# Kernel optimization log

Hardware: AMD Instinct MI355X
Metric: run time of the kernel (lower is better)

The kernel has to match this reference:

```python
import jax, jax.numpy as jnp
import numpy as np
import math


def setup_inputs() -> dict:
    key = jax.random.key(0)
    ks = jax.random.split(key, 6)
    B, C, H, W = 4, 384, 64, 64
    nd = 12
    d = C // nd  # 32 = projected channel width
    return {
        "x": jax.random.normal(ks[0], (B, C, H, W), jnp.float32),
        "xe": jax.random.normal(ks[1], (B, C, H, W), jnp.float32),
        "Wq": jax.random.normal(ks[2], (d, C), jnp.float32) * 0.02,      # 1x1 conv C -> d, no bias
        "Wkv": jax.random.normal(ks[3], (2 * d, C), jnp.float32) * 0.02,  # 1x1 conv C -> 2d, no bias
        "Wout": jax.random.normal(ks[4], (C, d, 3, 3), jnp.float32) * 0.02,  # 3x3 conv d -> C
        "bout": jnp.zeros((C,), jnp.float32),
        "n_div": 12,
    }


def reference(x, xe, Wq, Wkv, Wout, bout, n_div):
    B, C, H, W = x.shape
    Y, X = xe.shape[-2], xe.shape[-1]
    n_head = 1
    hd = C // (n_head * n_div)  # head_dim
    # 1x1 conv projections as einsums
    q = jnp.einsum('dc,bchw->bdhw', Wq, x).reshape(B, n_head, hd, H, W)
    kv = jnp.einsum('dc,bchw->bdhw', Wkv, xe).reshape(B, n_head, 2 * hd, Y, X)
    k, v = kv[:, :, :hd], kv[:, :, hd:]
    # full pairwise spatial attention scores [B, n_head, H, W, Y, X]
    scale = 1.0 / math.sqrt(C // n_div)
    attn = jnp.einsum('bnchw,bncyx->bnhwyx', q, k) * scale
    attn = jax.nn.softmax(attn.reshape(B, n_head, H, W, Y * X), axis=-1)
    attn = attn.reshape(B, n_head, H, W, Y, X)
    out = jnp.einsum('bnhwyx,bncyx->bnchw', attn, v).reshape(B, C // n_div, H, W)
    # 3x3 conv with padding 1, plus bias, then residual
    out = jax.lax.conv_general_dilated(
        out, Wout, window_strides=(1, 1), padding='SAME',
        dimension_numbers=('NCHW', 'OIHW', 'NCHW'))
    out = out + bout[None, :, None, None]
    return out + x
```

## Files before the change

kernel.cpp:

```cpp
#include <hip/hip_runtime.h>
#include <hip/hip_bf16.h>
#include <math.h>

#define B_   4
#define C_   384
#define HD_  32
#define P_   4096
#define PADP 4356
#define SCALE_ 0.17677669529663687f

typedef __attribute__((ext_vector_type(4))) float f32x4;
typedef __attribute__((ext_vector_type(8))) short short8;

static __device__ inline unsigned pk_bf16(float a, float b) {
    __hip_bfloat16 x = __float2bfloat16(a), y = __float2bfloat16(b);
    unsigned short ux = *reinterpret_cast<unsigned short*>(&x);
    unsigned short uy = *reinterpret_cast<unsigned short*>(&y);
    return (unsigned)ux | ((unsigned)uy << 16);
}
static __device__ inline short bf16_bits(float a) {
    __hip_bfloat16 x = __float2bfloat16(a);
    return *reinterpret_cast<short*>(&x);
}

__global__ void zero_kernel(f32x4* __restrict__ p, int n16) {
    int i = blockIdx.x * 256 + threadIdx.x;
    if (i < n16) p[i] = (f32x4){0.f, 0.f, 0.f, 0.f};
}

__global__ void repack_wproj_kernel(const float* __restrict__ Wq,
                                    const float* __restrict__ Wkv,
                                    short* __restrict__ Wball) {
    int idx = blockIdx.x * 256 + threadIdx.x;
    if (idx >= 96 * C_) return;
    int r = idx / C_, c = idx % C_;
    float v = (r < 32) ? Wq[r * C_ + c] : Wkv[(r - 32) * C_ + c];
    Wball[idx] = bf16_bits(v);
}

__global__ void repack_wconv_kernel(const float* __restrict__ Wout,
                                    short* __restrict__ Wbc) {
    int idx = blockIdx.x * 256 + threadIdx.x;
    if (idx >= 9 * 384 * 32) return;
    int ci = idx & 31;
    int co = (idx >> 5) % 384;
    int kk = idx / (384 * 32);
    int ky = kk / 3, kx = kk % 3;
    Wbc[idx] = bf16_bits(Wout[((co * 32 + ci) * 3 + ky) * 3 + kx]);
}

__global__ __launch_bounds__(256)
void transpose_kernel(const float* __restrict__ in, short* __restrict__ outT) {
    __shared__ float ls[64][65];
    int ct = blockIdx.x >> 6;
    int pt = blockIdx.x & 63;
    int b  = blockIdx.y;
    int c0 = ct << 6, p0 = pt << 6;
    int t = threadIdx.x;
    {
        int cc = t >> 2, pb = (t & 3) << 4;
        const float* src = in + ((size_t)b * C_ + c0 + cc) * P_ + p0 + pb;
        float4 v0 = *(const float4*)(src);
        float4 v1 = *(const float4*)(src + 4);
        float4 v2 = *(const float4*)(src + 8);
        float4 v3 = *(const float4*)(src + 12);
        float* d = &ls[cc][pb];
        d[0]=v0.x; d[1]=v0.y; d[2]=v0.z; d[3]=v0.w;
        d[4]=v1.x; d[5]=v1.y; d[6]=v1.z; d[7]=v1.w;
        d[8]=v2.x; d[9]=v2.y; d[10]=v2.z; d[11]=v2.w;
        d[12]=v3.x; d[13]=v3.y; d[14]=v3.z; d[15]=v3.w;
    }
    __syncthreads();
    {
        int p = t >> 2, cb = (t & 3) << 4;
        unsigned pkv[8];
        #pragma unroll
        for (int j = 0; j < 8; ++j)
            pkv[j] = pk_bf16(ls[cb + 2 * j][p], ls[cb + 2 * j + 1][p]);
        unsigned* dst = (unsigned*)(outT + ((size_t)b * P_ + p0 + p) * C_ + c0 + cb);
        #pragma unroll
        for (int j = 0; j < 8; ++j) dst[j] = pkv[j];
    }
}

__global__ __launch_bounds__(256)
void proj_gemm_kernel(const short* __restrict__ inT, const short* __restrict__ Wball,
                      short* __restrict__ pmOut, short* __restrict__ vOut, int role0) {
    int role = role0 + blockIdx.z;
    int b = blockIdx.y;
    int p0 = blockIdx.x << 6;
    int t = threadIdx.x, w = t >> 6, l = t & 63, lq = l & 15, h = l >> 4;
    int p = p0 + w * 16 + lq;
    const short* Ap = Wball + (size_t)(role * 32 + lq) * C_ + h * 8;
    const short* Bp = inT + ((size_t)b * P_ + p) * C_ + h * 8;
    f32x4 acc0 = {0.f,0.f,0.f,0.f}, acc1 = {0.f,0.f,0.f,0.f};
    short8 a0 = *(const short8*)(Ap);
    short8 a1 = *(const short8*)(Ap + 16 * C_);
    short8 bb = *(const short8*)(Bp);
    #pragma unroll
    for (int ks = 0; ks < 11; ++ks) {
        const short* Ap2 = Ap + (ks + 1) * 32;
        short8 na0 = *(const short8*)(Ap2);
        short8 na1 = *(const short8*)(Ap2 + 16 * C_);
        short8 nbb = *(const short8*)(Bp + (ks + 1) * 32);
        acc0 = __builtin_amdgcn_mfma_f32_16x16x32_bf16(a0, bb, acc0, 0, 0, 0);
        acc1 = __builtin_amdgcn_mfma_f32_16x16x32_bf16(a1, bb, acc1, 0, 0, 0);
        a0 = na0; a1 = na1; bb = nbb;
    }
    acc0 = __builtin_amdgcn_mfma_f32_16x16x32_bf16(a0, bb, acc0, 0, 0, 0);
    acc1 = __builtin_amdgcn_mfma_f32_16x16x32_bf16(a1, bb, acc1, 0, 0, 0);

    if (role < 2) {
        uint2 u0, u1;
        u0.x = pk_bf16(acc0[0], acc0[1]); u0.y = pk_bf16(acc0[2], acc0[3]);
        u1.x = pk_bf16(acc1[0], acc1[1]); u1.y = pk_bf16(acc1[2], acc1[3]);
        *(uint2*)(pmOut + ((size_t)b * P_ + p) * HD_ + h * 4)      = u0;
        *(uint2*)(pmOut + ((size_t)b * P_ + p) * HD_ + 16 + h * 4) = u1;
    } else {
        #pragma unroll
        for (int r = 0; r < 4; ++r) {
            vOut[((size_t)b * HD_ + h * 4 + r) * P_ + p]      = bf16_bits(acc0[r]);
            vOut[((size_t)b * HD_ + 16 + h * 4 + r) * P_ + p] = bf16_bits(acc1[r]);
        }
    }
}

__global__ __launch_bounds__(256, 4)
void attn_mfma_kernel(const short* __restrict__ qT,
                      const short* __restrict__ kT,
                      const short* __restrict__ vT,
                      short* __restrict__ aoT) {
    __shared__ unsigned p_lds[4][512];
    __shared__ float o_lds[4][32][16];
    __shared__ float m_lds[4][16], l_lds[4][16];

    int blk = blockIdx.x;
    int b = blk >> 8;
    int q0 = (blk & 255) << 4;
    int t = threadIdx.x;
    int w = t >> 6;
    int l = t & 63;
    int lq = l & 15;
    int h = l >> 4;

    const short* qTb = qT + ((size_t)b * P_ + q0) * HD_;
    const short* kTb = kT + (size_t)b * P_ * HD_;
    const short* vb  = vT + (size_t)b * HD_ * P_;

    short8 qf = *(const short8*)(qTb + lq * HD_ + h * 8);

    f32x4 o0 = {0.f,0.f,0.f,0.f}, o1 = {0.f,0.f,0.f,0.f};
    float m = -1e30f, lsum = 0.f;
    unsigned* myp = &p_lds[w][0];
    int swz = (lq & 7) << 4;

    int key_base = w * 1024;
    short8 kf[4], vf[4];
    {
        const short* kp = kTb + (size_t)(key_base + lq) * HD_ + h * 8;
        #pragma unroll
        for (int tt = 0; tt < 4; ++tt) kf[tt] = *(const short8*)(kp + tt * 16 * HD_);
        const short* vp = vb + (size_t)lq * P_ + key_base + h * 8;
        vf[0] = *(const short8*)(vp);
        vf[1] = *(const short8*)(vp + 32);
        vf[2] = *(const short8*)(vp + 16 * P_);
        vf[3] = *(const short8*)(vp + 16 * P_ + 32);
    }

    for (int kt = 0; kt < 16; ++kt) {
        short8 nk[4], nv[4];
        if (kt < 15) {
            int nxt = key_base + (kt + 1) * 64;
            const short* kp = kTb + (size_t)(nxt + lq) * HD_ + h * 8;
            #pragma unroll
            for (int tt = 0; tt < 4; ++tt) nk[tt] = *(const short8*)(kp + tt * 16 * HD_);
            const short* vp = vb + (size_t)lq * P_ + nxt + h * 8;
            nv[0] = *(const short8*)(vp);
            nv[1] = *(const short8*)(vp + 32);
            nv[2] = *(const short8*)(vp + 16 * P_);
            nv[3] = *(const short8*)(vp + 16 * P_ + 32);
        } else {
            #pragma unroll
            for (int tt = 0; tt < 4; ++tt) { nk[tt] = kf[tt]; nv[tt] = vf[tt]; }
        }

        f32x4 st[4];
        __builtin_amdgcn_s_setprio(1);
        #pragma unroll
        for (int tt = 0; tt < 4; ++tt)
            st[tt] = __builtin_amdgcn_mfma_f32_16x16x32_bf16(kf[tt], qf,
                         (f32x4){0.f,0.f,0.f,0.f}, 0, 0, 0);
        __builtin_amdgcn_s_setprio(0);

        float pm = -1e30f;
        #pragma unroll
        for (int tt = 0; tt < 4; ++tt)
            #pragma unroll
            for (int r = 0; r < 4; ++r) pm = fmaxf(pm, st[tt][r]);
        pm *= SCALE_;
        pm = fmaxf(pm, __shfl_xor(pm, 16));
        pm = fmaxf(pm, __shfl_xor(pm, 32));

        bool skip = __all(pm - m <= 8.0f);
        if (!skip) {
            float mnew = fmaxf(m, pm);
            float alpha = __expf(m - mnew);
            o0 *= alpha; o1 *= alpha;
            lsum *= alpha;
            m = mnew;
        }

        float rs = 0.f;
        unsigned pk[8];
        #pragma unroll
        for (int tt = 0; tt < 4; ++tt) {
            float p0e = __expf(st[tt][0] * SCALE_ - m);
            float p1e = __expf(st[tt][1] * SCALE_ - m);
            float p2e = __expf(st[tt][2] * SCALE_ - m);
            float p3e = __expf(st[tt][3] * SCALE_ - m);
            rs += p0e + p1e + p2e + p3e;
            pk[tt * 2 + 0] = pk_bf16(p0e, p1e);
            pk[tt * 2 + 1] = pk_bf16(p2e, p3e);
        }
        rs += __shfl_xor(rs, 16);
        rs += __shfl_xor(rs, 32);
        lsum += rs;

        #pragma unroll
        for (int tt = 0; tt < 4; ++tt) {
            int u0 = tt * 32 + h * 8;
            myp[(lq * 128 + ((u0 + 0) ^ swz)) >> 2] = pk[tt * 2 + 0];
            myp[(lq * 128 + ((u0 + 4) ^ swz)) >> 2] = pk[tt * 2 + 1];
        }
        short8 pb0, pb1;
        __builtin_memcpy(&pb0, (const char*)myp + lq * 128 + ((h * 16 + 0)  ^ swz), 16);
        __builtin_memcpy(&pb1, (const char*)myp + lq * 128 + ((h * 16 + 64) ^ swz), 16);

        __builtin_amdgcn_s_setprio(1);
        o0 = __builtin_amdgcn_mfma_f32_16x16x32_bf16(vf[0], pb0, o0, 0, 0, 0);
        o0 = __builtin_amdgcn_mfma_f32_16x16x32_bf16(vf[1], pb1, o0, 0, 0, 0);
        o1 = __builtin_amdgcn_mfma_f32_16x16x32_bf16(vf[2], pb0, o1, 0, 0, 0);
        o1 = __builtin_amdgcn_mfma_f32_16x16x32_bf16(vf[3], pb1, o1, 0, 0, 0);
        __builtin_amdgcn_s_setprio(0);

        #pragma unroll
        for (int tt = 0; tt < 4; ++tt) { kf[tt] = nk[tt]; vf[tt] = nv[tt]; }
    }

    #pragma unroll
    for (int r = 0; r < 4; ++r) {
        o_lds[w][h * 4 + r][lq]      = o0[r];
        o_lds[w][16 + h * 4 + r][lq] = o1[r];
    }
    if (h == 0) { m_lds[w][lq] = m; l_lds[w][lq] = lsum; }
    __syncthreads();

    {
        int qq = t >> 4;
        int d0 = (t & 15) * 2;
        float M = fmaxf(fmaxf(m_lds[0][qq], m_lds[1][qq]),
                        fmaxf(m_lds[2][qq], m_lds[3][qq]));
        float f[4]; float denom = 0.f;
        #pragma unroll
        for (int ww = 0; ww < 4; ++ww) {
            f[ww] = __expf(m_lds[ww][qq] - M);
            denom += l_lds[ww][qq] * f[ww];
        }
        float inv = 1.f / denom;
        float v0 = 0.f, v1 = 0.f;
        #pragma unroll
        for (int ww = 0; ww < 4; ++ww) {
            v0 += o_lds[ww][d0][qq] * f[ww];
            v1 += o_lds[ww][d0 + 1][qq] * f[ww];
        }
        int p = q0 + qq;
        int hh = p >> 6, ww2 = p & 63;
        unsigned* dst = (unsigned*)(aoT +
            ((size_t)b * PADP + (hh + 1) * 66 + (ww2 + 1)) * HD_ + d0);
        *dst = pk_bf16(v0 * inv, v1 * inv);
    }
}

__global__ __launch_bounds__(512)
void conv_mfma_kernel(const short* __restrict__ Wbc,
                      const short* __restrict__ aoT,
                      const float* __restrict__ bout,
                      const float* __restrict__ x,
                      float* __restrict__ out) {
    int blk = blockIdx.x;
    int b = blk >> 7;
    int p0 = (blk & 127) << 5;
    int t = threadIdx.x;
    int w = t >> 6, l = t & 63, lq = l & 15, h = l >> 4;
    int co0 = w * 48;

    const short* aob = aoT + (size_t)b * PADP * HD_;
    const short* bptr[2];
    #pragma unroll
    for (int n = 0; n < 2; ++n) {
        int p = p0 + n * 16 + lq;
        int hh = p >> 6, ww = p & 63;
        bptr[n] = aob + (size_t)(hh * 66 + ww) * HD_ + h * 8;
    }
    const short* aptr = Wbc + (size_t)(co0 + lq) * 32 + h * 8;

    f32x4 acc[3][2];
    #pragma unroll
    for (int m = 0; m < 3; ++m)
        #pragma unroll
        for (int n = 0; n < 2; ++n) acc[m][n] = (f32x4){0.f,0.f,0.f,0.f};

    short8 Bf0 = *(const short8*)(bptr[0]);
    short8 Bf1 = *(const short8*)(bptr[1]);
    #pragma unroll
    for (int kk = 0; kk < 9; ++kk) {
        short8 nB0, nB1;
        if (kk < 8) {
            int ky = (kk + 1) / 3, kx = (kk + 1) % 3;
            nB0 = *(const short8*)(bptr[0] + (ky * 66 + kx) * HD_);
            nB1 = *(const short8*)(bptr[1] + (ky * 66 + kx) * HD_);
        } else { nB0 = Bf0; nB1 = Bf1; }
        #pragma unroll
        for (int m = 0; m < 3; ++m) {
            short8 Af = *(const short8*)(aptr + kk * 12288 + m * 512);
            acc[m][0] = __builtin_amdgcn_mfma_f32_16x16x32_bf16(Af, Bf0, acc[m][0], 0, 0, 0);
            acc[m][1] = __builtin_amdgcn_mfma_f32_16x16x32_bf16(Af, Bf1, acc[m][1], 0, 0, 0);
        }
        Bf0 = nB0; Bf1 = nB1;
    }

    #pragma unroll
    for (int m = 0; m < 3; ++m) {
        #pragma unroll
        for (int r = 0; r < 4; ++r) {
            int co = co0 + m * 16 + h * 4 + r;
            float bias = bout[co];
            #pragma unroll
            for (int n = 0; n < 2; ++n) {
                int p = p0 + n * 16 + lq;
                size_t idx = ((size_t)b * C_ + co) * P_ + p;
                out[idx] = acc[m][n][r] + bias + x[idx];
            }
        }
    }
}

extern "C" void kernel_launch(void* const* d_in, const int* in_sizes, int n_in,
                              void* d_out, int out_size, void* d_ws, size_t ws_size,
                              hipStream_t stream) {
    const float* x    = (const float*)d_in[0];
    const float* xe   = (const float*)d_in[1];
    const float* Wq   = (const float*)d_in[2];
    const float* Wkv  = (const float*)d_in[3];
    const float* Wout = (const float*)d_in[4];
    const float* bout = (const float*)d_in[5];
    float* out = (float*)d_out;

    short* iT    = (short*)d_ws;
    short* qT    = iT    + (size_t)B_ * P_ * C_;
    short* kT    = qT    + (size_t)B_ * P_ * HD_;
    short* vT    = kT    + (size_t)B_ * P_ * HD_;
    short* aoT   = vT    + (size_t)B_ * P_ * HD_;
    short* Wball = aoT   + (size_t)B_ * PADP * HD_;
    short* Wbc   = Wball + 96 * C_;

    {
        int n16 = (B_ * PADP * HD_ * 2) / 16;
        zero_kernel<<<(n16 + 255) / 256, 256, 0, stream>>>((f32x4*)aoT, n16);
    }
    repack_wproj_kernel<<<(96 * C_ + 255) / 256, 256, 0, stream>>>(Wq, Wkv, Wball);
    repack_wconv_kernel<<<(9 * 384 * 32 + 255) / 256, 256, 0, stream>>>(Wout, Wbc);

    transpose_kernel<<<dim3(384, B_), 256, 0, stream>>>(xe, iT);
    proj_gemm_kernel<<<dim3(64, B_, 2), 256, 0, stream>>>(iT, Wball, kT, vT, 1);
    transpose_kernel<<<dim3(384, B_), 256, 0, stream>>>(x, iT);
    proj_gemm_kernel<<<dim3(64, B_, 1), 256, 0, stream>>>(iT, Wball, qT, vT, 0);

    attn_mfma_kernel<<<B_ * 256, 256, 0, stream>>>(qT, kT, vT, aoT);
    conv_mfma_kernel<<<B_ * 128, 512, 0, stream>>>(Wbc, aoT, bout, x, out);
}
```

Measured before the change: 108.4 us.

## Fuse projections into attention, drop transposes, use exp2 with prescaled Q

Removes the two fp32→bf16 transpose kernels. K/V are now projected straight from the NCHW input with strided loads and an in-register bf16 pack, and the Q projection is computed inside the attention kernel itself. The softmax scale and log2(e) are folded into Wq, so attention can use the raw v_exp_f32 (exp2) instruction. Attention moves to 8 waves per block with 32-key steps, split-K over 512 keys per wave, and keeps the row-sum local until the end. Several small launches are merged and only the padded border of aoT is zeroed, trading strided uncoalesced input reads and Q recomputation for less launch and memory traffic.

```diff
diff --git a/kernel.cpp b/kernel.cpp
--- a/kernel.cpp
+++ b/kernel.cpp
@@ -8,244 +8,201 @@
 #define P_   4096
 #define PADP 4356
 #define SCALE_ 0.17677669529663687f
+#define QSC_   0.2550889266f
 
 typedef __attribute__((ext_vector_type(4))) float f32x4;
 typedef __attribute__((ext_vector_type(8))) short short8;
 
-static __device__ inline unsigned pk_bf16(float a, float b) {
-    __hip_bfloat16 x = __float2bfloat16(a), y = __float2bfloat16(b);
-    unsigned short ux = *reinterpret_cast<unsigned short*>(&x);
-    unsigned short uy = *reinterpret_cast<unsigned short*>(&y);
-    return (unsigned)ux | ((unsigned)uy << 16);
+static __device__ inline unsigned cvt_pk(float lo, float hi) {
+    unsigned r;
+    asm("v_cvt_pk_bf16_f32 %0, %1, %2" : "=v"(r) : "v"(lo), "v"(hi));
+    return r;
+}
+static __device__ inline float exp2a(float x) {
+    float r;
+    asm("v_exp_f32 %0, %1" : "=v"(r) : "v"(x));
+    return r;
 }
 static __device__ inline short bf16_bits(float a) {
     __hip_bfloat16 x = __float2bfloat16(a);
     return *reinterpret_cast<short*>(&x);
 }
 
-__global__ void zero_kernel(f32x4* __restrict__ p, int n16) {
-    int i = blockIdx.x * 256 + threadIdx.x;
-    if (i < n16) p[i] = (f32x4){0.f, 0.f, 0.f, 0.f};
-}
-
-__global__ void repack_wproj_kernel(const float* __restrict__ Wq,
-                                    const float* __restrict__ Wkv,
-                                    short* __restrict__ Wball) {
+__global__ void border_zero_kernel(unsigned* __restrict__ aoT32) {
     int idx = blockIdx.x * 256 + threadIdx.x;
-    if (idx >= 96 * C_) return;
-    int r = idx / C_, c = idx % C_;
-    float v = (r < 32) ? Wq[r * C_ + c] : Wkv[(r - 32) * C_ + c];
-    Wball[idx] = bf16_bits(v);
-}
-
-__global__ void repack_wconv_kernel(const float* __restrict__ Wout,
-                                    short* __restrict__ Wbc) {
+    if (idx >= B_ * 260 * 16) return;
+    int j = idx & 15;
+    int p = (idx >> 4) % 260;
+    int b = idx / (260 * 16);
+    int hh, ww;
+    if (p < 66)       { hh = 0;  ww = p; }
+    else if (p < 132) { hh = 65; ww = p - 66; }
+    else { int i = p - 132; hh = 1 + (i >> 1); ww = (i & 1) * 65; }
+    aoT32[((size_t)b * PADP + hh * 66 + ww) * 16 + j] = 0;
+}
+
+__global__ void repack_kernel(const float* __restrict__ Wq,
+                              const float* __restrict__ Wkv,
+                              const float* __restrict__ Wout,
+                              short* __restrict__ Wball,
+                              short* __restrict__ Wbc) {
     int idx = blockIdx.x * 256 + threadIdx.x;
-    if (idx >= 9 * 384 * 32) return;
-    int ci = idx & 31;
-    int co = (idx >> 5) % 384;
-    int kk = idx / (384 * 32);
-    int ky = kk / 3, kx = kk % 3;
-    Wbc[idx] = bf16_bits(Wout[((co * 32 + ci) * 3 + ky) * 3 + kx]);
-}
-
-__global__ __launch_bounds__(256)
-void transpose_kernel(const float* __restrict__ in, short* __restrict__ outT) {
-    __shared__ float ls[64][65];
-    int ct = blockIdx.x >> 6;
-    int pt = blockIdx.x & 63;
-    int b  = blockIdx.y;
-    int c0 = ct << 6, p0 = pt << 6;
-    int t = threadIdx.x;
-    {
-        int cc = t >> 2, pb = (t & 3) << 4;
-        const float* src = in + ((size_t)b * C_ + c0 + cc) * P_ + p0 + pb;
-        float4 v0 = *(const float4*)(src);
-        float4 v1 = *(const float4*)(src + 4);
-        float4 v2 = *(const float4*)(src + 8);
-        float4 v3 = *(const float4*)(src + 12);
-        float* d = &ls[cc][pb];
-        d[0]=v0.x; d[1]=v0.y; d[2]=v0.z; d[3]=v0.w;
-        d[4]=v1.x; d[5]=v1.y; d[6]=v1.z; d[7]=v1.w;
-        d[8]=v2.x; d[9]=v2.y; d[10]=v2.z; d[11]=v2.w;
-        d[12]=v3.x; d[13]=v3.y; d[14]=v3.z; d[15]=v3.w;
-    }
-    __syncthreads();
-    {
-        int p = t >> 2, cb = (t & 3) << 4;
-        unsigned pkv[8];
-        #pragma unroll
-        for (int j = 0; j < 8; ++j)
-            pkv[j] = pk_bf16(ls[cb + 2 * j][p], ls[cb + 2 * j + 1][p]);
-        unsigned* dst = (unsigned*)(outT + ((size_t)b * P_ + p0 + p) * C_ + c0 + cb);
-        #pragma unroll
-        for (int j = 0; j < 8; ++j) dst[j] = pkv[j];
-    }
-}
-
-__global__ __launch_bounds__(256)
-void proj_gemm_kernel(const short* __restrict__ inT, const short* __restrict__ Wball,
-                      short* __restrict__ pmOut, short* __restrict__ vOut, int role0) {
-    int role = role0 + blockIdx.z;
+    if (idx < 96 * C_) {
+        int r = idx / C_, c = idx % C_;
+        float v = (r < 32) ? Wq[r * C_ + c] * QSC_ : Wkv[(r - 32) * C_ + c];
+        Wball[idx] = bf16_bits(v);
+    }
+    int j = idx - 96 * C_;
+    if (j >= 0 && j < 9 * 384 * 32) {
+        int ci = j & 31;
+        int co = (j >> 5) % 384;
+        int kk = j / (384 * 32);
+        int ky = kk / 3, kx = kk % 3;
+        Wbc[j] = bf16_bits(Wout[((co * 32 + ci) * 3 + ky) * 3 + kx]);
+    }
+}
+
+__global__ __launch_bounds__(512)
+void proj_kv_kernel(const float* __restrict__ xe, const short* __restrict__ Wball,
+                    short* __restrict__ kT, short* __restrict__ vT) {
     int b = blockIdx.y;
-    int p0 = blockIdx.x << 6;
+    int p0 = blockIdx.x << 5;
     int t = threadIdx.x, w = t >> 6, l = t & 63, lq = l & 15, h = l >> 4;
-    int p = p0 + w * 16 + lq;
-    const short* Ap = Wball + (size_t)(role * 32 + lq) * C_ + h * 8;
-    const short* Bp = inT + ((size_t)b * P_ + p) * C_ + h * 8;
-    f32x4 acc0 = {0.f,0.f,0.f,0.f}, acc1 = {0.f,0.f,0.f,0.f};
-    short8 a0 = *(const short8*)(Ap);
-    short8 a1 = *(const short8*)(Ap + 16 * C_);
-    short8 bb = *(const short8*)(Bp);
-    #pragma unroll
-    for (int ks = 0; ks < 11; ++ks) {
-        const short* Ap2 = Ap + (ks + 1) * 32;
-        short8 na0 = *(const short8*)(Ap2);
-        short8 na1 = *(const short8*)(Ap2 + 16 * C_);
-        short8 nbb = *(const short8*)(Bp + (ks + 1) * 32);
-        acc0 = __builtin_amdgcn_mfma_f32_16x16x32_bf16(a0, bb, acc0, 0, 0, 0);
-        acc1 = __builtin_amdgcn_mfma_f32_16x16x32_bf16(a1, bb, acc1, 0, 0, 0);
-        a0 = na0; a1 = na1; bb = nbb;
-    }
-    acc0 = __builtin_amdgcn_mfma_f32_16x16x32_bf16(a0, bb, acc0, 0, 0, 0);
-    acc1 = __builtin_amdgcn_mfma_f32_16x16x32_bf16(a1, bb, acc1, 0, 0, 0);
-
-    if (role < 2) {
-        uint2 u0, u1;
-        u0.x = pk_bf16(acc0[0], acc0[1]); u0.y = pk_bf16(acc0[2], acc0[3]);
-        u1.x = pk_bf16(acc1[0], acc1[1]); u1.y = pk_bf16(acc1[2], acc1[3]);
-        *(uint2*)(pmOut + ((size_t)b * P_ + p) * HD_ + h * 4)      = u0;
-        *(uint2*)(pmOut + ((size_t)b * P_ + p) * HD_ + 16 + h * 4) = u1;
+    int mt = w >> 1, pg = w & 1;
+    int p = p0 + pg * 16 + lq;
+    const float* xb = xe + (size_t)b * C_ * P_ + p;
+    const short* Ap = Wball + (size_t)(32 + mt * 16 + lq) * C_ + h * 8;
+    f32x4 acc = {0.f, 0.f, 0.f, 0.f};
+    for (int ks = 0; ks < 12; ++ks) {
+        float xv[8];
+        #pragma unroll
+        for (int jj = 0; jj < 8; ++jj)
+            xv[jj] = xb[(size_t)(ks * 32 + h * 8 + jj) * P_];
+        unsigned u[4];
+        #pragma unroll
+        for (int jj = 0; jj < 4; ++jj) u[jj] = cvt_pk(xv[2 * jj], xv[2 * jj + 1]);
+        short8 bf;
+        __builtin_memcpy(&bf, u, 16);
+        short8 af = *(const short8*)(Ap + ks * 32);
+        acc = __builtin_amdgcn_mfma_f32_16x16x32_bf16(af, bf, acc, 0, 0, 0);
+    }
+    if (mt < 2) {
+        uint2 u;
+        u.x = cvt_pk(acc[0], acc[1]);
+        u.y = cvt_pk(acc[2], acc[3]);
+        *(uint2*)(kT + ((size_t)b * P_ + p) * HD_ + mt * 16 + h * 4) = u;
     } else {
-        #pragma unroll
-        for (int r = 0; r < 4; ++r) {
-            vOut[((size_t)b * HD_ + h * 4 + r) * P_ + p]      = bf16_bits(acc0[r]);
-            vOut[((size_t)b * HD_ + 16 + h * 4 + r) * P_ + p] = bf16_bits(acc1[r]);
-        }
-    }
-}
-
-__global__ __launch_bounds__(256, 4)
-void attn_mfma_kernel(const short* __restrict__ qT,
-                      const short* __restrict__ kT,
-                      const short* __restrict__ vT,
+        int d = (mt - 2) * 16 + h * 4;
+        #pragma unroll
+        for (int r = 0; r < 4; ++r)
+            vT[((size_t)b * HD_ + d + r) * P_ + p] = bf16_bits(acc[r]);
+    }
+}
+
+__global__ __launch_bounds__(512, 8)
+void attn_mfma_kernel(const float* __restrict__ x, const short* __restrict__ Wball,
+                      const short* __restrict__ kT, const short* __restrict__ vT,
                       short* __restrict__ aoT) {
-    __shared__ unsigned p_lds[4][512];
-    __shared__ float o_lds[4][32][16];
-    __shared__ float m_lds[4][16], l_lds[4][16];
+    __shared__ unsigned p_lds[8][256];
+    __shared__ float o_lds[8][32][16];
+    __shared__ float m_lds[8][16], l_lds[8][16];
 
     int blk = blockIdx.x;
     int b = blk >> 8;
     int q0 = (blk & 255) << 4;
-    int t = threadIdx.x;
-    int w = t >> 6;
-    int l = t & 63;
-    int lq = l & 15;
-    int h = l >> 4;
-
-    const short* qTb = qT + ((size_t)b * P_ + q0) * HD_;
+    int t = threadIdx.x, w = t >> 6, l = t & 63, lq = l & 15, h = l >> 4;
+    unsigned* myp = &p_lds[w][0];
+
+    short8 qf;
+    {
+        const float* xb = x + (size_t)b * C_ * P_ + q0 + lq;
+        const short* A0 = Wball + (size_t)lq * C_ + h * 8;
+        f32x4 qa0 = {0.f, 0.f, 0.f, 0.f}, qa1 = {0.f, 0.f, 0.f, 0.f};
+        for (int ks = 0; ks < 12; ++ks) {
+            float xv[8];
+            #pragma unroll
+            for (int jj = 0; jj < 8; ++jj)
+                xv[jj] = xb[(size_t)(ks * 32 + h * 8 + jj) * P_];
+            unsigned u[4];
+            #pragma unroll
+            for (int jj = 0; jj < 4; ++jj) u[jj] = cvt_pk(xv[2 * jj], xv[2 * jj + 1]);
+            short8 bf;
+            __builtin_memcpy(&bf, u, 16);
+            short8 a0 = *(const short8*)(A0 + ks * 32);
+            short8 a1 = *(const short8*)(A0 + 16 * C_ + ks * 32);
+            qa0 = __builtin_amdgcn_mfma_f32_16x16x32_bf16(a0, bf, qa0, 0, 0, 0);
+            qa1 = __builtin_amdgcn_mfma_f32_16x16x32_bf16(a1, bf, qa1, 0, 0, 0);
+        }
+        uint2 u0, u1;
+        u0.x = cvt_pk(qa0[0], qa0[1]); u0.y = cvt_pk(qa0[2], qa0[3]);
+        u1.x = cvt_pk(qa1[0], qa1[1]); u1.y = cvt_pk(qa1[2], qa1[3]);
+        *(uint2*)((char*)myp + lq * 64 + h * 8)      = u0;
+        *(uint2*)((char*)myp + lq * 64 + 32 + h * 8) = u1;
+        __builtin_memcpy(&qf, (const char*)myp + lq * 64 + h * 16, 16);
+    }
+
     const short* kTb = kT + (size_t)b * P_ * HD_;
     const short* vb  = vT + (size_t)b * HD_ * P_;
-
-    short8 qf = *(const short8*)(qTb + lq * HD_ + h * 8);
-
-    f32x4 o0 = {0.f,0.f,0.f,0.f}, o1 = {0.f,0.f,0.f,0.f};
+    int key_base = w * 512;
+    int swzB = ((lq >> 1) & 3) << 4;
+
+    f32x4 o0 = {0.f, 0.f, 0.f, 0.f}, o1 = {0.f, 0.f, 0.f, 0.f};
     float m = -1e30f, lsum = 0.f;
-    unsigned* myp = &p_lds[w][0];
-    int swz = (lq & 7) << 4;
-
-    int key_base = w * 1024;
-    short8 kf[4], vf[4];
-    {
-        const short* kp = kTb + (size_t)(key_base + lq) * HD_ + h * 8;
-        #pragma unroll
-        for (int tt = 0; tt < 4; ++tt) kf[tt] = *(const short8*)(kp + tt * 16 * HD_);
-        const short* vp = vb + (size_t)lq * P_ + key_base + h * 8;
-        vf[0] = *(const short8*)(vp);
-        vf[1] = *(const short8*)(vp + 32);
-        vf[2] = *(const short8*)(vp + 16 * P_);
-        vf[3] = *(const short8*)(vp + 16 * P_ + 32);
-    }
+
+    const short* kp0 = kTb + (size_t)(key_base + lq) * HD_ + h * 8;
+    short8 k0 = *(const short8*)(kp0);
+    short8 k1 = *(const short8*)(kp0 + 16 * HD_);
 
     for (int kt = 0; kt < 16; ++kt) {
-        short8 nk[4], nv[4];
-        if (kt < 15) {
-            int nxt = key_base + (kt + 1) * 64;
-            const short* kp = kTb + (size_t)(nxt + lq) * HD_ + h * 8;
-            #pragma unroll
-            for (int tt = 0; tt < 4; ++tt) nk[tt] = *(const short8*)(kp + tt * 16 * HD_);
-            const short* vp = vb + (size_t)lq * P_ + nxt + h * 8;
-            nv[0] = *(const short8*)(vp);
-            nv[1] = *(const short8*)(vp + 32);
-            nv[2] = *(const short8*)(vp + 16 * P_);
-            nv[3] = *(const short8*)(vp + 16 * P_ + 32);
-        } else {
-            #pragma unroll
-            for (int tt = 0; tt < 4; ++tt) { nk[tt] = kf[tt]; nv[tt] = vf[tt]; }
-        }
-
-        f32x4 st[4];
-        __builtin_amdgcn_s_setprio(1);
-        #pragma unroll
-        for (int tt = 0; tt < 4; ++tt)
-            st[tt] = __builtin_amdgcn_mfma_f32_16x16x32_bf16(kf[tt], qf,
-                         (f32x4){0.f,0.f,0.f,0.f}, 0, 0, 0);
-        __builtin_amdgcn_s_setprio(0);
-
-        float pm = -1e30f;
-        #pragma unroll
-        for (int tt = 0; tt < 4; ++tt)
-            #pragma unroll
-            for (int r = 0; r < 4; ++r) pm = fmaxf(pm, st[tt][r]);
-        pm *= SCALE_;
+        int key0 = key_base + kt * 32;
+        f32x4 s0 = __builtin_amdgcn_mfma_f32_16x16x32_bf16(k0, qf,
+                       (f32x4){0.f, 0.f, 0.f, 0.f}, 0, 0, 0);
+        f32x4 s1 = __builtin_amdgcn_mfma_f32_16x16x32_bf16(k1, qf,
+                       (f32x4){0.f, 0.f, 0.f, 0.f}, 0, 0, 0);
+
+        int nxt = key0 + (kt < 15 ? 32 : 0);
+        const short* kp = kTb + (size_t)(nxt + lq) * HD_ + h * 8;
+        short8 nk0 = *(const short8*)(kp);
+        short8 nk1 = *(const short8*)(kp + 16 * HD_);
+
+        const short* vp = vb + (size_t)lq * P_ + key0 + h * 8;
+        short8 va0 = *(const short8*)(vp);
+        short8 va1 = *(const short8*)(vp + 16 * P_);
+
+        float pm = fmaxf(fmaxf(fmaxf(s0[0], s0[1]), fmaxf(s0[2], s0[3])),
+                         fmaxf(fmaxf(s1[0], s1[1]), fmaxf(s1[2], s1[3])));
         pm = fmaxf(pm, __shfl_xor(pm, 16));
         pm = fmaxf(pm, __shfl_xor(pm, 32));
-
-        bool skip = __all(pm - m <= 8.0f);
-        if (!skip) {
+        if (!__all(pm - m <= 8.0f)) {
             float mnew = fmaxf(m, pm);
-            float alpha = __expf(m - mnew);
-            o0 *= alpha; o1 *= alpha;
-            lsum *= alpha;
+            float alpha = exp2a(m - mnew);
+            o0 *= alpha; o1 *= alpha; lsum *= alpha;
             m = mnew;
         }
-
-        float rs = 0.f;
-        unsigned pk[8];
-        #pragma unroll
-        for (int tt = 0; tt < 4; ++tt) {
-            float p0e = __expf(st[tt][0] * SCALE_ - m);
-            float p1e = __expf(st[tt][1] * SCALE_ - m);
-            float p2e = __expf(st[tt][2] * SCALE_ - m);
-            float p3e = __expf(st[tt][3] * SCALE_ - m);
-            rs += p0e + p1e + p2e + p3e;
-            pk[tt * 2 + 0] = pk_bf16(p0e, p1e);
-            pk[tt * 2 + 1] = pk_bf16(p2e, p3e);
-        }
-        rs += __shfl_xor(rs, 16);
-        rs += __shfl_xor(rs, 32);
-        lsum += rs;
-
-        #pragma unroll
-        for (int tt = 0; tt < 4; ++tt) {
-            int u0 = tt * 32 + h * 8;
-            myp[(lq * 128 + ((u0 + 0) ^ swz)) >> 2] = pk[tt * 2 + 0];
-            myp[(lq * 128 + ((u0 + 4) ^ swz)) >> 2] = pk[tt * 2 + 1];
-        }
-        short8 pb0, pb1;
-        __builtin_memcpy(&pb0, (const char*)myp + lq * 128 + ((h * 16 + 0)  ^ swz), 16);
-        __builtin_memcpy(&pb1, (const char*)myp + lq * 128 + ((h * 16 + 64) ^ swz), 16);
+        float e0 = exp2a(s0[0] - m), e1 = exp2a(s0[1] - m);
+        float e2 = exp2a(s0[2] - m), e3 = exp2a(s0[3] - m);
+        float e4 = exp2a(s1[0] - m), e5 = exp2a(s1[1] - m);
+        float e6 = exp2a(s1[2] - m), e7 = exp2a(s1[3] - m);
+        lsum += ((e0 + e1) + (e2 + e3)) + ((e4 + e5) + (e6 + e7));
+
+        uint2 w0, w1;
+        w0.x = cvt_pk(e0, e1); w0.y = cvt_pk(e2, e3);
+        w1.x = cvt_pk(e4, e5); w1.y = cvt_pk(e6, e7);
+        *(uint2*)((char*)myp + lq * 64 + ((h * 8) ^ swzB))      = w0;
+        *(uint2*)((char*)myp + lq * 64 + ((32 + h * 8) ^ swzB)) = w1;
+        short8 pb;
+        __builtin_memcpy(&pb, (const char*)myp + lq * 64 + ((h * 16) ^ swzB), 16);
 
         __builtin_amdgcn_s_setprio(1);
-        o0 = __builtin_amdgcn_mfma_f32_16x16x32_bf16(vf[0], pb0, o0, 0, 0, 0);
-        o0 = __builtin_amdgcn_mfma_f32_16x16x32_bf16(vf[1], pb1, o0, 0, 0, 0);
-        o1 = __builtin_amdgcn_mfma_f32_16x16x32_bf16(vf[2], pb0, o1, 0, 0, 0);
-        o1 = __builtin_amdgcn_mfma_f32_16x16x32_bf16(vf[3], pb1, o1, 0, 0, 0);
+        o0 = __builtin_amdgcn_mfma_f32_16x16x32_bf16(va0, pb, o0, 0, 0, 0);
+        o1 = __builtin_amdgcn_mfma_f32_16x16x32_bf16(va1, pb, o1, 0, 0, 0);
         __builtin_amdgcn_s_setprio(0);
 
-        #pragma unroll
-        for (int tt = 0; tt < 4; ++tt) { kf[tt] = nk[tt]; vf[tt] = nv[tt]; }
-    }
+        k0 = nk0; k1 = nk1;
+    }
+
+    lsum += __shfl_xor(lsum, 16);
+    lsum += __shfl_xor(lsum, 32);
 
     #pragma unroll
     for (int r = 0; r < 4; ++r) {
@@ -255,29 +212,26 @@
     if (h == 0) { m_lds[w][lq] = m; l_lds[w][lq] = lsum; }
     __syncthreads();
 
-    {
+    if (t < 256) {
         int qq = t >> 4;
         int d0 = (t & 15) * 2;
-        float M = fmaxf(fmaxf(m_lds[0][qq], m_lds[1][qq]),
-                        fmaxf(m_lds[2][qq], m_lds[3][qq]));
-        float f[4]; float denom = 0.f;
-        #pragma unroll
-        for (int ww = 0; ww < 4; ++ww) {
-            f[ww] = __expf(m_lds[ww][qq] - M);
-            denom += l_lds[ww][qq] * f[ww];
+        float M = -1e30f;
+        #pragma unroll
+        for (int ww = 0; ww < 8; ++ww) M = fmaxf(M, m_lds[ww][qq]);
+        float denom = 0.f, v0 = 0.f, v1 = 0.f;
+        #pragma unroll
+        for (int ww = 0; ww < 8; ++ww) {
+            float f = exp2a(m_lds[ww][qq] - M);
+            denom += l_lds[ww][qq] * f;
+            v0 += o_lds[ww][d0][qq] * f;
+            v1 += o_lds[ww][d0 + 1][qq] * f;
         }
         float inv = 1.f / denom;
-        float v0 = 0.f, v1 = 0.f;
-        #pragma unroll
-        for (int ww = 0; ww < 4; ++ww) {
-            v0 += o_lds[ww][d0][qq] * f[ww];
-            v1 += o_lds[ww][d0 + 1][qq] * f[ww];
-        }
         int p = q0 + qq;
         int hh = p >> 6, ww2 = p & 63;
         unsigned* dst = (unsigned*)(aoT +
             ((size_t)b * PADP + (hh + 1) * 66 + (ww2 + 1)) * HD_ + d0);
-        *dst = pk_bf16(v0 * inv, v1 * inv);
+        *dst = cvt_pk(v0 * inv, v1 * inv);
     }
 }
 
@@ -308,7 +262,7 @@
     #pragma unroll
     for (int m = 0; m < 3; ++m)
         #pragma unroll
-        for (int n = 0; n < 2; ++n) acc[m][n] = (f32x4){0.f,0.f,0.f,0.f};
+        for (int n = 0; n < 2; ++n) acc[m][n] = (f32x4){0.f, 0.f, 0.f, 0.f};
 
     short8 Bf0 = *(const short8*)(bptr[0]);
     short8 Bf1 = *(const short8*)(bptr[1]);
@@ -356,26 +310,16 @@
     const float* bout = (const float*)d_in[5];
     float* out = (float*)d_out;
 
-    short* iT    = (short*)d_ws;
-    short* qT    = iT    + (size_t)B_ * P_ * C_;
-    short* kT    = qT    + (size_t)B_ * P_ * HD_;
-    short* vT    = kT    + (size_t)B_ * P_ * HD_;
-    short* aoT   = vT    + (size_t)B_ * P_ * HD_;
-    short* Wball = aoT   + (size_t)B_ * PADP * HD_;
+    short* kT    = (short*)d_ws;
+    short* vT    = kT  + (size_t)B_ * P_ * HD_;
+    short* aoT   = vT  + (size_t)B_ * P_ * HD_;
+    short* Wball = aoT + (size_t)B_ * PADP * HD_;
     short* Wbc   = Wball + 96 * C_;
 
-    {
-        int n16 = (B_ * PADP * HD_ * 2) / 16;
-        zero_kernel<<<(n16 + 255) / 256, 256, 0, stream>>>((f32x4*)aoT, n16);
-    }
-    repack_wproj_kernel<<<(96 * C_ + 255) / 256, 256, 0, stream>>>(Wq, Wkv, Wball);
-    repack_wconv_kernel<<<(9 * 384 * 32 + 255) / 256, 256, 0, stream>>>(Wout, Wbc);
-
-    transpose_kernel<<<dim3(384, B_), 256, 0, stream>>>(xe, iT);
-    proj_gemm_kernel<<<dim3(64, B_, 2), 256, 0, stream>>>(iT, Wball, kT, vT, 1);
-    transpose_kernel<<<dim3(384, B_), 256, 0, stream>>>(x, iT);
-    proj_gemm_kernel<<<dim3(64, B_, 1), 256, 0, stream>>>(iT, Wball, qT, vT, 0);
-
-    attn_mfma_kernel<<<B_ * 256, 256, 0, stream>>>(qT, kT, vT, aoT);
+    border_zero_kernel<<<(B_ * 260 * 16 + 255) / 256, 256, 0, stream>>>((unsigned*)aoT);
+    repack_kernel<<<(96 * C_ + 9 * 384 * 32 + 255) / 256, 256, 0, stream>>>(
+        Wq, Wkv, Wout, Wball, Wbc);
+    proj_kv_kernel<<<dim3(128, B_), 512, 0, stream>>>(xe, Wball, kT, vT);
+    attn_mfma_kernel<<<B_ * 256, 512, 0, stream>>>(x, Wball, kT, vT, aoT);
     conv_mfma_kernel<<<B_ * 128, 512, 0, stream>>>(Wbc, aoT, bout, x, out);
 }
```

Measured after the change: 113.0 us. +4.3%, slower.
